# Kernel optimization log

Measured on AMD Instinct MI355X. Metric: run time of the kernel, lower is better.

## Reference

```python
import jax, jax.numpy as jnp
import numpy as np

D_MODEL = 2048
D_FF = 8192


def absmean_quant(w):
    # scale = mean(|w|); keep weights whose magnitude >= 0.7*scale, ternarize to {-1,0,1}
    scale = jnp.mean(jnp.abs(w))
    mask = (jnp.abs(w) >= scale * 0.7).astype(w.dtype)
    return jnp.sign(w) * mask


def setup_inputs() -> dict:
    key = jax.random.key(0)
    k_x, k_w1, k_w2 = jax.random.split(key, 3)
    x = jax.random.normal(k_x, (4, 4096, D_MODEL), dtype=jnp.float32)
    w1 = jax.random.normal(k_w1, (D_FF, D_MODEL), dtype=jnp.float32)  # fc1.weight
    b1 = jnp.zeros((D_FF,), dtype=jnp.float32)
    w2 = jax.random.normal(k_w2, (D_MODEL, D_FF), dtype=jnp.float32)  # fc2.weight
    b2 = jnp.zeros((D_MODEL,), dtype=jnp.float32)
    return {"x": x, "w1": w1, "b1": b1, "w2": w2, "b2": b2}


def reference(x, w1, b1, w2, b2):
    w1_q = absmean_quant(w1)
    w2_q = absmean_quant(w2)
    h = jnp.einsum('bsd,fd->bsf', x, w1_q) + b1  # fc1: [B,S,d_ff]
    h = jax.nn.gelu(h, approximate=False)        # torch nn.GELU default = exact erf
    out = jnp.einsum('bsf,df->bsd', h, w2_q) + b2  # fc2: [B,S,d_model]
    return out
```

## Files before the change

kernel.cpp:

```cpp
#include <hip/hip_runtime.h>
#include <hip/hip_bf16.h>
#include <math.h>
#include <stdint.h>

#define D_MODEL 2048
#define D_FF    8192
#define MTOK    16384
#define NW      (D_FF * D_MODEL)

typedef int    i32x4  __attribute__((ext_vector_type(4)));
typedef __bf16 bf16x8 __attribute__((ext_vector_type(8)));

#define GLOAD_LDS16(gp, lp)                                                   \
  __builtin_amdgcn_global_load_lds(                                           \
      (__attribute__((address_space(1))) void*)(gp),                          \
      (__attribute__((address_space(3))) void*)(lp), 16, 0, 0)

__global__ void absum_s1(const float* __restrict__ w1, const float* __restrict__ w2,
                         double* __restrict__ partials) {
    const float* w = blockIdx.y ? w2 : w1;
    __shared__ double sm[256];
    int tid = blockIdx.x * 256 + threadIdx.x;
    double s = 0.0;
    for (int i = tid; i < NW / 4; i += 1024 * 256) {
        float4 v = ((const float4*)w)[i];
        s += (double)fabsf(v.x) + (double)fabsf(v.y) + (double)fabsf(v.z) + (double)fabsf(v.w);
    }
    sm[threadIdx.x] = s;
    __syncthreads();
    for (int off = 128; off > 0; off >>= 1) {
        if (threadIdx.x < off) sm[threadIdx.x] += sm[threadIdx.x + off];
        __syncthreads();
    }
    if (threadIdx.x == 0) partials[blockIdx.y * 1024 + blockIdx.x] = sm[0];
}

__global__ void absum_s2(const double* __restrict__ partials, float* __restrict__ thr) {
    __shared__ double sm[256];
    for (int wsel = 0; wsel < 2; ++wsel) {
        const double* p = partials + wsel * 1024;
        double s = p[threadIdx.x] + p[threadIdx.x + 256] + p[threadIdx.x + 512] + p[threadIdx.x + 768];
        sm[threadIdx.x] = s;
        __syncthreads();
        for (int off = 128; off > 0; off >>= 1) {
            if (threadIdx.x < off) sm[threadIdx.x] += sm[threadIdx.x + off];
            __syncthreads();
        }
        if (threadIdx.x == 0) thr[wsel] = (float)(0.7 * (sm[0] / (double)NW));
        __syncthreads();
    }
}

__global__ void quantw1(const float* __restrict__ w, const float* __restrict__ thr,
                        int8_t* __restrict__ q) {
    float t = thr[0];
    int i = (blockIdx.x * 256 + threadIdx.x) * 4;
    float4 v = *(const float4*)(w + i);
    char4 o;
    o.x = (fabsf(v.x) >= t) ? (v.x > 0.f ? 1 : -1) : 0;
    o.y = (fabsf(v.y) >= t) ? (v.y > 0.f ? 1 : -1) : 0;
    o.z = (fabsf(v.z) >= t) ? (v.z > 0.f ? 1 : -1) : 0;
    o.w = (fabsf(v.w) >= t) ? (v.w > 0.f ? 1 : -1) : 0;
    *(char4*)(q + i) = o;
}

__global__ void quantw2(const float* __restrict__ w, const float* __restrict__ thr,
                        int8_t* __restrict__ q, float* __restrict__ colsum) {
    __shared__ int sm[256];
    float t = thr[1];
    const int row = blockIdx.x;
    const int tid = threadIdx.x;
    int isum = 0;
    #pragma unroll
    for (int j = 0; j < 8; ++j) {
        int idx = row * D_FF + j * 1024 + tid * 4;
        float4 v = *(const float4*)(w + idx);
        char4 o;
        o.x = (fabsf(v.x) >= t) ? (v.x > 0.f ? 1 : -1) : 0;
        o.y = (fabsf(v.y) >= t) ? (v.y > 0.f ? 1 : -1) : 0;
        o.z = (fabsf(v.z) >= t) ? (v.z > 0.f ? 1 : -1) : 0;
        o.w = (fabsf(v.w) >= t) ? (v.w > 0.f ? 1 : -1) : 0;
        isum += o.x + o.y + o.z + o.w;
        *(char4*)(q + idx) = o;
    }
    sm[tid] = isum;
    __syncthreads();
    for (int off = 128; off > 0; off >>= 1) {
        if (tid < off) sm[tid] += sm[tid + off];
        __syncthreads();
    }
    if (tid == 0) colsum[row] = (float)sm[0];
}

__global__ void xquant(const float* __restrict__ x, int8_t* __restrict__ xq,
                       float* __restrict__ sx) {
    __shared__ float sm[256];
    const int row = blockIdx.x;
    const int tid = threadIdx.x;
    float4 v[2];
    float mx = 0.f;
    #pragma unroll
    for (int j = 0; j < 2; ++j) {
        v[j] = *(const float4*)(x + (size_t)row * D_MODEL + j * 1024 + tid * 4);
        mx = fmaxf(mx, fmaxf(fmaxf(fabsf(v[j].x), fabsf(v[j].y)),
                             fmaxf(fabsf(v[j].z), fabsf(v[j].w))));
    }
    sm[tid] = mx;
    __syncthreads();
    for (int off = 128; off > 0; off >>= 1) {
        if (tid < off) sm[tid] = fmaxf(sm[tid], sm[tid + off]);
        __syncthreads();
    }
    float m = sm[0];
    float inv = (m > 0.f) ? 127.f / m : 0.f;
    if (tid == 0) sx[row] = (m > 0.f) ? m / 127.f : 0.f;
    #pragma unroll
    for (int j = 0; j < 2; ++j) {
        char4 o;
        o.x = (int8_t)min(127, max(-127, __float2int_rn(v[j].x * inv)));
        o.y = (int8_t)min(127, max(-127, __float2int_rn(v[j].y * inv)));
        o.z = (int8_t)min(127, max(-127, __float2int_rn(v[j].z * inv)));
        o.w = (int8_t)min(127, max(-127, __float2int_rn(v[j].w * inv)));
        *(char4*)(xq + (size_t)row * D_MODEL + j * 1024 + tid * 4) = o;
    }
}

__global__ void hquant(const __bf16* __restrict__ h, int8_t* __restrict__ hq,
                       float2* __restrict__ sh) {
    __shared__ float sm[256];
    const int row = blockIdx.x;
    const int tid = threadIdx.x;
    const float gmin = -0.17f;
    float vals[4][8];
    float mx = -1e30f;
    #pragma unroll
    for (int j = 0; j < 4; ++j) {
        bf16x8 b = *(const bf16x8*)(h + (size_t)row * D_FF + j * 2048 + tid * 8);
        #pragma unroll
        for (int e = 0; e < 8; ++e) {
            float f = (float)b[e];
            vals[j][e] = f;
            mx = fmaxf(mx, f);
        }
    }
    sm[tid] = mx;
    __syncthreads();
    for (int off = 128; off > 0; off >>= 1) {
        if (tid < off) sm[tid] = fmaxf(sm[tid], sm[tid + off]);
        __syncthreads();
    }
    float M = sm[0];
    float s = (M - gmin) / 254.f;
    float inv = 254.f / (M - gmin);
    if (tid == 0) sh[row] = make_float2(s, 127.f * s + gmin);
    #pragma unroll
    for (int j = 0; j < 4; ++j) {
        char4 o0, o1;
        int q[8];
        #pragma unroll
        for (int e = 0; e < 8; ++e)
            q[e] = min(127, max(-127, __float2int_rn((vals[j][e] - gmin) * inv) - 127));
        o0.x = q[0]; o0.y = q[1]; o0.z = q[2]; o0.w = q[3];
        o1.x = q[4]; o1.y = q[5]; o1.z = q[6]; o1.w = q[7];
        int8_t* p = hq + (size_t)row * D_FF + j * 2048 + tid * 8;
        *(char4*)p = o0;
        *(char4*)(p + 4) = o1;
    }
}

template<int EPI>
__global__ __launch_bounds__(256, 2) void gemm_i8_bt(
    const int8_t* __restrict__ A,
    const int8_t* __restrict__ B,
    const float*  __restrict__ bias,
    const float*  __restrict__ rs,
    const float*  __restrict__ colsum,
    void* __restrict__ Cout,
    int M, int N, int K)
{
    __shared__ int8_t Sh[3 * 24576];

    const int tid  = threadIdx.x;
    const int wave = tid >> 6;
    const int lane = tid & 63;
    const int quad = lane >> 4;
    const int l15  = lane & 15;
    const int wm   = (wave >> 1) * 128;
    const int wn   = (wave & 1) * 64;

    const int gx   = gridDim.x;
    const int orig = blockIdx.y * gx + blockIdx.x;
    const int xcd  = orig & 7;
    const int l    = orig >> 3;
    const int stsh = (EPI == 0) ? 8 : 6;
    const int st   = l >> stsh;
    const int r    = l & ((1 << stsh) - 1);
    const int by   = xcd * 8 + st * 4 + (r & 3);
    const int bx   = r >> 2;
    const int m0 = by << 8;
    const int n0 = bx << 7;

    i32x4 acc[8][4] = {};

    const int8_t* gA[4]; const int8_t* gB[2];
    #pragma unroll
    for (int it = 0; it < 4; ++it) {
        int slot = it * 256 + tid;
        int row  = slot >> 2;
        int cg   = (slot & 3) ^ ((row >> 1) & 3);
        gA[it] = A + (size_t)(m0 + row) * K + cg * 16;
    }
    #pragma unroll
    for (int it = 0; it < 2; ++it) {
        int slot = it * 256 + tid;
        int row  = slot >> 2;
        int cg   = (slot & 3) ^ ((row >> 1) & 3);
        gB[it] = B + (size_t)(n0 + row) * K + cg * 16;
    }
    char* const ldsb = (char*)Sh;
    char* dA[4]; char* dB[2];
    #pragma unroll
    for (int it = 0; it < 4; ++it) dA[it] = ldsb + it * 4096 + wave * 1024;
    #pragma unroll
    for (int it = 0; it < 2; ++it) dB[it] = ldsb + 16384 + it * 4096 + wave * 1024;

    int aoff[8], boff[4];
    #pragma unroll
    for (int f = 0; f < 8; ++f) {
        int ra = wm + f * 16 + l15;
        aoff[f] = ra * 64 + ((quad ^ ((ra >> 1) & 3)) << 4);
    }
    #pragma unroll
    for (int f = 0; f < 4; ++f) {
        int rb = wn + f * 16 + l15;
        boff[f] = 16384 + rb * 64 + ((quad ^ ((rb >> 1) & 3)) << 4);
    }

    const int NH = K >> 6;
    const int STG = 24576;

    #pragma unroll
    for (int h = 0; h < 2; ++h) {
        #pragma unroll
        for (int it = 0; it < 4; ++it) { GLOAD_LDS16(gA[it], dA[it] + h * STG); gA[it] += 64; }
        #pragma unroll
        for (int it = 0; it < 2; ++it) { GLOAD_LDS16(gB[it], dB[it] + h * STG); gB[it] += 64; }
    }
    asm volatile("s_waitcnt vmcnt(6)" ::: "memory");
    __builtin_amdgcn_s_barrier();
    __builtin_amdgcn_sched_barrier(0);

    int roff = 0;
    int soff = 2 * STG;

    for (int s = 0; s < NH; ++s) {
        if (s + 2 < NH) {
            #pragma unroll
            for (int it = 0; it < 4; ++it) { GLOAD_LDS16(gA[it], dA[it] + soff); gA[it] += 64; }
            #pragma unroll
            for (int it = 0; it < 2; ++it) { GLOAD_LDS16(gB[it], dB[it] + soff); gB[it] += 64; }
        }
        i32x4 bfr[4], afr[8];
        #pragma unroll
        for (int f = 0; f < 4; ++f) bfr[f] = *(const i32x4*)(ldsb + roff + boff[f]);
        #pragma unroll
        for (int f = 0; f < 8; ++f) afr[f] = *(const i32x4*)(ldsb + roff + aoff[f]);
        __builtin_amdgcn_s_setprio(1);
        #pragma unroll
        for (int mf = 0; mf < 8; ++mf)
            #pragma unroll
            for (int nf = 0; nf < 4; ++nf)
                acc[mf][nf] = __builtin_amdgcn_mfma_i32_16x16x64_i8(
                    afr[mf], bfr[nf], acc[mf][nf], 0, 0, 0);
        __builtin_amdgcn_s_setprio(0);
        if (s < NH - 2)       { asm volatile("s_waitcnt vmcnt(6)" ::: "memory"); }
        else if (s == NH - 2) { asm volatile("s_waitcnt vmcnt(0)" ::: "memory"); }
        __builtin_amdgcn_sched_barrier(0);
        __builtin_amdgcn_s_barrier();
        __builtin_amdgcn_sched_barrier(0);
        roff = (roff == 2 * STG) ? 0 : roff + STG;
        soff = (soff == 2 * STG) ? 0 : soff + STG;
    }

    #pragma unroll
    for (int nf = 0; nf < 4; ++nf) {
        const int n = n0 + wn + nf * 16 + l15;
        const float bv = bias[n];
        const float cs = (EPI == 1) ? colsum[n] : 0.f;
        #pragma unroll
        for (int mf = 0; mf < 8; ++mf)
            #pragma unroll
            for (int r = 0; r < 4; ++r) {
                int m = m0 + wm + mf * 16 + quad * 4 + r;
                float a = (float)acc[mf][nf][r];
                if (EPI == 0) {
                    float v = rs[m] * a + bv;
                    v = 0.5f * v * (1.0f + erff(v * 0.70710678118654752f));
                    ((__bf16*)Cout)[(size_t)m * N + n] = (__bf16)v;
                } else {
                    float2 so = ((const float2*)rs)[m];
                    ((float*)Cout)[(size_t)m * N + n] = so.x * a + so.y * cs + bv;
                }
            }
    }
}

extern "C" void kernel_launch(void* const* d_in, const int* in_sizes, int n_in,
                              void* d_out, int out_size, void* d_ws, size_t ws_size,
                              hipStream_t stream) {
    const float* x  = (const float*)d_in[0];
    const float* w1 = (const float*)d_in[1];
    const float* b1 = (const float*)d_in[2];
    const float* w2 = (const float*)d_in[3];
    const float* b2 = (const float*)d_in[4];
    float* out = (float*)d_out;

    char* ws = (char*)d_ws;
    float*  thr = (float*)ws;
    float*  sx  = (float*)(ws + 256);
    float2* sh  = (float2*)(ws + 256 + (64 << 10));
    float*  colsum = (float*)(ws + 256 + (192 << 10));
    int8_t* xq  = (int8_t*)(ws + 256 + (256 << 10));
    int8_t* w1q = xq  + (size_t)MTOK * D_MODEL;
    int8_t* w2q = w1q + (size_t)D_FF * D_MODEL;
    int8_t* hq  = w2q + (size_t)D_MODEL * D_FF;
    __bf16* h   = (__bf16*)(hq + (size_t)MTOK * D_FF);
    double* partials = (double*)h;

    absum_s1<<<dim3(1024, 2), 256, 0, stream>>>(w1, w2, partials);
    absum_s2<<<1, 256, 0, stream>>>(partials, thr);

    quantw1<<<NW / 1024, 256, 0, stream>>>(w1, thr, w1q);
    quantw2<<<D_MODEL, 256, 0, stream>>>(w2, thr, w2q, colsum);
    xquant<<<MTOK, 256, 0, stream>>>(x, xq, sx);

    dim3 g1(D_FF / 128, MTOK / 256);
    gemm_i8_bt<0><<<g1, 256, 0, stream>>>(xq, w1q, b1, sx, nullptr, (void*)h,
                                          MTOK, D_FF, D_MODEL);

    hquant<<<MTOK, 256, 0, stream>>>(h, hq, sh);

    dim3 g2(D_MODEL / 128, MTOK / 256);
    gemm_i8_bt<1><<<g2, 256, 0, stream>>>(hq, w2q, b2, (const float*)sh, colsum, (void*)out,
                                          MTOK, D_MODEL, D_FF);
}
```

Before: 1.138 ms.

## Shrink GEMM tile to 128x128, deepen LDS ring, prefetch fragments, stage bf16 epilogue

The int8 GEMM tile drops from 256x128 to 128x128, the LDS ring grows from 3 to 4 stages, and the A/B fragments for the next k-step are read from LDS ahead of time into registers while the current MFMAs run. The fc1 epilogue now writes the GELU bf16 output through padded LDS so global stores are coalesced 16-byte rows. The aim is more blocks, more latency hiding and wider stores. In exchange each block does less reuse per byte loaded, so global and LDS traffic per MFMA goes up. The block-to-tile swizzle is also changed to match the doubled grid height.

```diff
diff --git a/kernel.cpp b/kernel.cpp
--- a/kernel.cpp
+++ b/kernel.cpp
@@ -178,14 +178,14 @@
     void* __restrict__ Cout,
     int M, int N, int K)
 {
-    __shared__ int8_t Sh[3 * 24576];
+    __shared__ int8_t Sh[4 * 16384];
 
     const int tid  = threadIdx.x;
     const int wave = tid >> 6;
     const int lane = tid & 63;
     const int quad = lane >> 4;
     const int l15  = lane & 15;
-    const int wm   = (wave >> 1) * 128;
+    const int wm   = (wave >> 1) * 64;
     const int wn   = (wave & 1) * 64;
 
     const int gx   = gridDim.x;
@@ -195,113 +195,137 @@
     const int stsh = (EPI == 0) ? 8 : 6;
     const int st   = l >> stsh;
     const int r    = l & ((1 << stsh) - 1);
-    const int by   = xcd * 8 + st * 4 + (r & 3);
+    const int by   = xcd * 16 + st * 4 + (r & 3);
     const int bx   = r >> 2;
-    const int m0 = by << 8;
+    const int m0 = by << 7;
     const int n0 = bx << 7;
 
-    i32x4 acc[8][4] = {};
-
-    const int8_t* gA[4]; const int8_t* gB[2];
-    #pragma unroll
-    for (int it = 0; it < 4; ++it) {
+    i32x4 acc[4][4] = {};
+
+    const int8_t* gA[2]; const int8_t* gB[2];
+    char* dA[2]; char* dB[2];
+    char* const ldsb = (char*)Sh;
+    #pragma unroll
+    for (int it = 0; it < 2; ++it) {
         int slot = it * 256 + tid;
         int row  = slot >> 2;
         int cg   = (slot & 3) ^ ((row >> 1) & 3);
         gA[it] = A + (size_t)(m0 + row) * K + cg * 16;
-    }
-    #pragma unroll
-    for (int it = 0; it < 2; ++it) {
-        int slot = it * 256 + tid;
-        int row  = slot >> 2;
-        int cg   = (slot & 3) ^ ((row >> 1) & 3);
         gB[it] = B + (size_t)(n0 + row) * K + cg * 16;
-    }
-    char* const ldsb = (char*)Sh;
-    char* dA[4]; char* dB[2];
-    #pragma unroll
-    for (int it = 0; it < 4; ++it) dA[it] = ldsb + it * 4096 + wave * 1024;
-    #pragma unroll
-    for (int it = 0; it < 2; ++it) dB[it] = ldsb + 16384 + it * 4096 + wave * 1024;
-
-    int aoff[8], boff[4];
-    #pragma unroll
-    for (int f = 0; f < 8; ++f) {
+        dA[it] = ldsb + it * 4096 + wave * 1024;
+        dB[it] = ldsb + 8192 + it * 4096 + wave * 1024;
+    }
+
+    int aoff[4], boff[4];
+    #pragma unroll
+    for (int f = 0; f < 4; ++f) {
         int ra = wm + f * 16 + l15;
         aoff[f] = ra * 64 + ((quad ^ ((ra >> 1) & 3)) << 4);
-    }
-    #pragma unroll
-    for (int f = 0; f < 4; ++f) {
         int rb = wn + f * 16 + l15;
-        boff[f] = 16384 + rb * 64 + ((quad ^ ((rb >> 1) & 3)) << 4);
+        boff[f] = 8192 + rb * 64 + ((quad ^ ((rb >> 1) & 3)) << 4);
     }
 
     const int NH = K >> 6;
-    const int STG = 24576;
-
-    #pragma unroll
-    for (int h = 0; h < 2; ++h) {
-        #pragma unroll
-        for (int it = 0; it < 4; ++it) { GLOAD_LDS16(gA[it], dA[it] + h * STG); gA[it] += 64; }
-        #pragma unroll
-        for (int it = 0; it < 2; ++it) { GLOAD_LDS16(gB[it], dB[it] + h * STG); gB[it] += 64; }
-    }
-    asm volatile("s_waitcnt vmcnt(6)" ::: "memory");
+    const int STG = 16384;
+
+    #pragma unroll
+    for (int h = 0; h < 3; ++h) {
+        #pragma unroll
+        for (int it = 0; it < 2; ++it) {
+            GLOAD_LDS16(gA[it], dA[it] + h * STG);
+            GLOAD_LDS16(gB[it], dB[it] + h * STG);
+            gA[it] += 64; gB[it] += 64;
+        }
+    }
+    asm volatile("s_waitcnt vmcnt(4)" ::: "memory");
     __builtin_amdgcn_s_barrier();
     __builtin_amdgcn_sched_barrier(0);
 
-    int roff = 0;
-    int soff = 2 * STG;
+    i32x4 af[4], bfr[4];
+    #pragma unroll
+    for (int f = 0; f < 4; ++f) {
+        af[f]  = *(const i32x4*)(ldsb + aoff[f]);
+        bfr[f] = *(const i32x4*)(ldsb + boff[f]);
+    }
 
     for (int s = 0; s < NH; ++s) {
-        if (s + 2 < NH) {
-            #pragma unroll
-            for (int it = 0; it < 4; ++it) { GLOAD_LDS16(gA[it], dA[it] + soff); gA[it] += 64; }
-            #pragma unroll
-            for (int it = 0; it < 2; ++it) { GLOAD_LDS16(gB[it], dB[it] + soff); gB[it] += 64; }
-        }
-        i32x4 bfr[4], afr[8];
-        #pragma unroll
-        for (int f = 0; f < 4; ++f) bfr[f] = *(const i32x4*)(ldsb + roff + boff[f]);
-        #pragma unroll
-        for (int f = 0; f < 8; ++f) afr[f] = *(const i32x4*)(ldsb + roff + aoff[f]);
+        const int roff_n = ((s + 1) & 3) * STG;
+        const int soff   = ((s + 3) & 3) * STG;
+        if (s + 3 < NH) {
+            #pragma unroll
+            for (int it = 0; it < 2; ++it) {
+                GLOAD_LDS16(gA[it], ldsb + soff + (dA[it] - ldsb));
+                GLOAD_LDS16(gB[it], ldsb + soff + (dB[it] - ldsb));
+                gA[it] += 64; gB[it] += 64;
+            }
+        }
+        i32x4 afn[4], bfn[4];
+        if (s + 1 < NH) {
+            #pragma unroll
+            for (int f = 0; f < 4; ++f) {
+                afn[f] = *(const i32x4*)(ldsb + roff_n + aoff[f]);
+                bfn[f] = *(const i32x4*)(ldsb + roff_n + boff[f]);
+            }
+        }
         __builtin_amdgcn_s_setprio(1);
         #pragma unroll
-        for (int mf = 0; mf < 8; ++mf)
+        for (int mf = 0; mf < 4; ++mf)
             #pragma unroll
             for (int nf = 0; nf < 4; ++nf)
                 acc[mf][nf] = __builtin_amdgcn_mfma_i32_16x16x64_i8(
-                    afr[mf], bfr[nf], acc[mf][nf], 0, 0, 0);
+                    af[mf], bfr[nf], acc[mf][nf], 0, 0, 0);
         __builtin_amdgcn_s_setprio(0);
-        if (s < NH - 2)       { asm volatile("s_waitcnt vmcnt(6)" ::: "memory"); }
-        else if (s == NH - 2) { asm volatile("s_waitcnt vmcnt(0)" ::: "memory"); }
-        __builtin_amdgcn_sched_barrier(0);
+        #pragma unroll
+        for (int f = 0; f < 4; ++f) { af[f] = afn[f]; bfr[f] = bfn[f]; }
+        if (s < NH - 1) {
+            __builtin_amdgcn_sched_barrier(0);
+            if (s + 3 < NH) { asm volatile("s_waitcnt vmcnt(4)" ::: "memory"); }
+            else            { asm volatile("s_waitcnt vmcnt(0)" ::: "memory"); }
+            __builtin_amdgcn_s_barrier();
+            __builtin_amdgcn_sched_barrier(0);
+        }
+    }
+
+    if (EPI == 0) {
         __builtin_amdgcn_s_barrier();
-        __builtin_amdgcn_sched_barrier(0);
-        roff = (roff == 2 * STG) ? 0 : roff + STG;
-        soff = (soff == 2 * STG) ? 0 : soff + STG;
-    }
-
-    #pragma unroll
-    for (int nf = 0; nf < 4; ++nf) {
-        const int n = n0 + wn + nf * 16 + l15;
-        const float bv = bias[n];
-        const float cs = (EPI == 1) ? colsum[n] : 0.f;
-        #pragma unroll
-        for (int mf = 0; mf < 8; ++mf)
-            #pragma unroll
-            for (int r = 0; r < 4; ++r) {
-                int m = m0 + wm + mf * 16 + quad * 4 + r;
-                float a = (float)acc[mf][nf][r];
-                if (EPI == 0) {
-                    float v = rs[m] * a + bv;
+        char* Cs = ldsb;
+        #pragma unroll
+        for (int nf = 0; nf < 4; ++nf) {
+            const int n = n0 + wn + nf * 16 + l15;
+            const float bv = bias[n];
+            #pragma unroll
+            for (int mf = 0; mf < 4; ++mf)
+                #pragma unroll
+                for (int r = 0; r < 4; ++r) {
+                    int mloc = wm + mf * 16 + quad * 4 + r;
+                    float v = rs[m0 + mloc] * (float)acc[mf][nf][r] + bv;
                     v = 0.5f * v * (1.0f + erff(v * 0.70710678118654752f));
-                    ((__bf16*)Cout)[(size_t)m * N + n] = (__bf16)v;
-                } else {
+                    *(__bf16*)(Cs + mloc * 272 + (wn + nf * 16 + l15) * 2) = (__bf16)v;
+                }
+        }
+        __builtin_amdgcn_s_barrier();
+        const int rr = tid >> 1, hh = tid & 1;
+        const char* src = Cs + rr * 272 + hh * 128;
+        __bf16* dst = (__bf16*)Cout + (size_t)(m0 + rr) * N + n0 + hh * 64;
+        #pragma unroll
+        for (int j = 0; j < 8; ++j)
+            *(i32x4*)(dst + j * 8) = *(const i32x4*)(src + j * 16);
+    } else {
+        #pragma unroll
+        for (int nf = 0; nf < 4; ++nf) {
+            const int n = n0 + wn + nf * 16 + l15;
+            const float bv = bias[n];
+            const float cs = colsum[n];
+            #pragma unroll
+            for (int mf = 0; mf < 4; ++mf)
+                #pragma unroll
+                for (int r = 0; r < 4; ++r) {
+                    int m = m0 + wm + mf * 16 + quad * 4 + r;
                     float2 so = ((const float2*)rs)[m];
-                    ((float*)Cout)[(size_t)m * N + n] = so.x * a + so.y * cs + bv;
+                    ((float*)Cout)[(size_t)m * N + n] =
+                        so.x * (float)acc[mf][nf][r] + so.y * cs + bv;
                 }
-            }
+        }
     }
 }
 
@@ -334,13 +358,13 @@
     quantw2<<<D_MODEL, 256, 0, stream>>>(w2, thr, w2q, colsum);
     xquant<<<MTOK, 256, 0, stream>>>(x, xq, sx);
 
-    dim3 g1(D_FF / 128, MTOK / 256);
+    dim3 g1(D_FF / 128, MTOK / 128);
     gemm_i8_bt<0><<<g1, 256, 0, stream>>>(xq, w1q, b1, sx, nullptr, (void*)h,
                                           MTOK, D_FF, D_MODEL);
 
     hquant<<<MTOK, 256, 0, stream>>>(h, hq, sh);
 
-    dim3 g2(D_MODEL / 128, MTOK / 256);
+    dim3 g2(D_MODEL / 128, MTOK / 128);
     gemm_i8_bt<1><<<g2, 256, 0, stream>>>(hq, w2q, b2, (const float*)sh, colsum, (void*)out,
                                           MTOK, D_MODEL, D_FF);
 }
```

Result: slower. 1.223 ms (+7.4%).
